# Optimization experiments

Hardware: AMD Instinct MI355X
Metric: run time of the kernel (lower is better)

Reference implementation:

```python
import jax, jax.numpy as jnp
import numpy as np

K = 3          # kernel size
STRIDE = 1
PAD = 1
GROUPS = 32    # GroupNorm groups
EPS = 1e-5


def setup_inputs() -> dict:
    key = jax.random.key(0)
    ks = jax.random.split(key, 6)
    B, Cin, H, W, Cout = 4, 256, 64, 64, 256
    K2 = K * K
    x = jax.random.normal(ks[0], (B, Cin, H, W), jnp.float32)
    offset = jax.random.normal(ks[1], (B, 2 * K2, H, W), jnp.float32)
    mask = jax.random.uniform(ks[2], (B, K2, H, W), jnp.float32)
    weight = jax.random.normal(ks[3], (Cout, Cin, K, K), jnp.float32) * (1.0 / np.sqrt(Cin * K2))
    bias = jnp.zeros((Cout,), jnp.float32)
    gamma = jnp.ones((Cout,), jnp.float32)   # constant_init(norm, 1)
    beta = jnp.zeros((Cout,), jnp.float32)   # bias=0
    return {"x": x, "offset": offset, "mask": mask, "weight": weight,
            "bias": bias, "gamma": gamma, "beta": beta}


def _modulated_deform_conv(x, offset, mask, weight, bias):
    """DCNv2: bilinear-sample x at learned offsets, modulate by mask, conv-accumulate."""
    B, Cin, H, W = x.shape
    Cout = weight.shape[0]
    K2 = K * K
    Ho = (H + 2 * PAD - K) // STRIDE + 1
    Wo = (W + 2 * PAD - K) // STRIDE + 1

    # base sampling grid per kernel point: [K2, Ho, Wo]
    ky, kx = jnp.meshgrid(jnp.arange(K), jnp.arange(K), indexing='ij')
    ky = ky.reshape(K2).astype(jnp.float32)
    kx = kx.reshape(K2).astype(jnp.float32)
    hs = (jnp.arange(Ho) * STRIDE - PAD).astype(jnp.float32)
    ws = (jnp.arange(Wo) * STRIDE - PAD).astype(jnp.float32)

    off = offset.reshape(B, K2, 2, Ho, Wo)  # interleaved (dy, dx) per kernel point
    y = ky[None, :, None, None] + hs[None, None, :, None] + off[:, :, 0]   # [B,K2,Ho,Wo]
    xc = kx[None, :, None, None] + ws[None, None, None, :] + off[:, :, 1]  # [B,K2,Ho,Wo]

    y0 = jnp.floor(y)
    x0 = jnp.floor(xc)
    dy = y - y0
    dx = xc - x0
    y0i = y0.astype(jnp.int32)
    x0i = x0.astype(jnp.int32)

    x_flat = x.reshape(B, Cin, H * W)

    def corner(yi, xi, w):
        # corner-wise zero padding outside the image (matches mmcv bilinear)
        valid = (yi >= 0) & (yi <= H - 1) & (xi >= 0) & (xi <= W - 1)
        idx = jnp.clip(yi, 0, H - 1) * W + jnp.clip(xi, 0, W - 1)  # [B,K2,Ho,Wo]
        idx_f = idx.reshape(B, -1)
        v = jax.vmap(lambda xf, i: xf[:, i])(x_flat, idx_f)  # [B, Cin, K2*Ho*Wo]
        wv = (w * valid.astype(w.dtype)).reshape(B, 1, -1)
        return v * wv

    val = (corner(y0i,     x0i,     (1 - dy) * (1 - dx))
         + corner(y0i,     x0i + 1, (1 - dy) * dx)
         + corner(y0i + 1, x0i,     dy * (1 - dx))
         + corner(y0i + 1, x0i + 1, dy * dx))
    val = val.reshape(B, Cin, K2, Ho, Wo) * mask[:, None]  # modulate

    w_r = weight.reshape(Cout, Cin, K2)
    out = jnp.einsum('bckhw,ock->bohw', val, w_r) + bias[None, :, None, None]
    return out


def _group_norm(x, gamma, beta):
    B, C, H, W = x.shape
    g = x.reshape(B, GROUPS, C // GROUPS, H, W)
    mu = g.mean(axis=(2, 3, 4), keepdims=True)
    var = ((g - mu) ** 2).mean(axis=(2, 3, 4), keepdims=True)
    g = (g - mu) * jax.lax.rsqrt(var + EPS)
    return g.reshape(B, C, H, W) * gamma[None, :, None, None] + beta[None, :, None, None]


def reference(x, offset, mask, weight, bias, gamma, beta):
    out = _modulated_deform_conv(x, offset, mask, weight, bias)
    out = _group_norm(out, gamma, beta)
    return jax.nn.relu(out)
```

## Files before the change

kernel.cpp:

```cpp
#include <hip/hip_runtime.h>
#include <math.h>

#define BB    4
#define CIN   256
#define HH    64
#define WWID  64
#define COUT  256
#define KKS   3
#define K2    9
#define PADV  1
#define HWSZ  4096
#define GROUPS 32
#define CPG   8
#define EPSV  1e-5f
#define KTOT  2304
#define ROWB  4608
#define NTOT  16384
#define NCHUNK 18

typedef __attribute__((ext_vector_type(8))) short bf16x8;
typedef __attribute__((ext_vector_type(4))) float f32x4;

#define GLOAD_LDS16(g, l) \
    __builtin_amdgcn_global_load_lds((const __attribute__((address_space(1))) unsigned int*)(g), \
                                     (__attribute__((address_space(3))) unsigned int*)(l), 16, 0, 0)

__device__ __forceinline__ unsigned short f2bf(float f) {
    unsigned u = __float_as_uint(f);
    u = (u + 0x7fffu + ((u >> 16) & 1u)) >> 16;
    return (unsigned short)u;
}
__device__ __forceinline__ float bflo(unsigned q) { return __uint_as_float(q << 16); }
__device__ __forceinline__ float bfhi(unsigned q) { return __uint_as_float(q & 0xffff0000u); }

__global__ __launch_bounds__(256)
void k_pre(const float* __restrict__ x, unsigned short* __restrict__ xh,
           const float* __restrict__ w, unsigned short* __restrict__ wtb,
           float* __restrict__ gstat) {
    int t = threadIdx.x;
    if (blockIdx.x < 128) {
        __shared__ float tile[32][33];
        int hw0 = blockIdx.x * 32;
        int c0  = blockIdx.y * 32;
        int b   = blockIdx.z;
        int tx = t & 31, ty = t >> 5;
        const float* xp = x + (size_t)b * CIN * HWSZ;
        #pragma unroll
        for (int i = 0; i < 4; i++)
            tile[ty + i * 8][tx] = xp[(c0 + ty + i * 8) * HWSZ + hw0 + tx];
        __syncthreads();
        int j = t >> 3, cq = t & 7;
        union { unsigned short s[4]; uint2 d; } pk;
        #pragma unroll
        for (int k = 0; k < 4; k++) pk.s[k] = f2bf(tile[cq * 4 + k][j]);
        *(uint2*)((char*)xh + ((size_t)b * HWSZ * CIN + (size_t)(hw0 + j) * CIN + c0 + cq * 4) * 2) = pk.d;
    } else {
        if (blockIdx.y == 0 && blockIdx.z == 0 && t < BB * GROUPS * 2) gstat[t] = 0.f;
        int idx = (blockIdx.y * 4 + blockIdx.z) * 256 + t;
        int co = idx >> 5, c8 = idx & 31;
        int cin0 = c8 * 8;
        for (int k2 = 0; k2 < K2; k2++) {
            union { unsigned short s[8]; uint4 q; } pk;
            #pragma unroll
            for (int j = 0; j < 8; j++)
                pk.s[j] = f2bf(w[(co * CIN + cin0 + j) * K2 + k2]);
            int phys = co * ROWB + k2 * 512 + (c8 >> 3) * 128 + ((c8 & 7) ^ (co & 7)) * 16;
            *(uint4*)((char*)wtb + phys) = pk.q;
        }
    }
}

__global__ __launch_bounds__(256)
void k_sample(const unsigned short* __restrict__ xh,
              const float* __restrict__ offset, const float* __restrict__ mask,
              unsigned short* __restrict__ val) {
    __shared__ int   cidx[16 * K2 * 4];
    __shared__ float cwgt[16 * K2 * 4];
    int n0 = blockIdx.x * 16;
    int b  = n0 >> 12;
    int t  = threadIdx.x;

    if (t < 16 * K2) {
        int p  = t / K2, k2 = t - p * K2;
        int hw = (n0 & 4095) + p;
        int ho = hw >> 6, wo = hw & 63;
        int ky = k2 / KKS, kx = k2 - ky * KKS;
        float dy = offset[((b * (2 * K2) + k2 * 2 + 0) * HWSZ) + hw];
        float dx = offset[((b * (2 * K2) + k2 * 2 + 1) * HWSZ) + hw];
        float m  = mask[(b * K2 + k2) * HWSZ + hw];
        float y  = (float)(ky + ho - PADV) + dy;
        float xc = (float)(kx + wo - PADV) + dx;
        float y0f = floorf(y), x0f = floorf(xc);
        float fy = y - y0f, fx = xc - x0f;
        int y0 = (int)y0f, x0 = (int)x0f;
        int   yy[2] = { y0, y0 + 1 };
        int   xx[2] = { x0, x0 + 1 };
        float wy[2] = { 1.f - fy, fy };
        float wx[2] = { 1.f - fx, fx };
        int base = t * 4;
        #pragma unroll
        for (int i = 0; i < 2; i++)
            #pragma unroll
            for (int j = 0; j < 2; j++) {
                int yi = yy[i], xi = xx[j];
                bool valid = (yi >= 0) && (yi < HH) && (xi >= 0) && (xi < WWID);
                int yc  = min(max(yi, 0), HH - 1);
                int xcc = min(max(xi, 0), WWID - 1);
                cidx[base + i * 2 + j] = yc * WWID + xcc;
                cwgt[base + i * 2 + j] = valid ? (wy[i] * wx[j] * m) : 0.f;
            }
    }
    __syncthreads();

    int c8 = t & 31, ps = t >> 5;
    const char* xb = (const char*)xh + (size_t)b * HWSZ * CIN * 2;
    #pragma unroll
    for (int i = 0; i < 2; i++) {
        int p = ps + 8 * i;
        int n = n0 + p;
        int skey = n & 7;
        for (int k2 = 0; k2 < K2; k2++) {
            int cb = (p * K2 + k2) * 4;
            float a0=0,a1=0,a2=0,a3=0,a4=0,a5=0,a6=0,a7=0;
            #pragma unroll
            for (int cor = 0; cor < 4; cor++) {
                float wv = cwgt[cb + cor];
                uint4 q = *(const uint4*)(xb + (size_t)cidx[cb + cor] * 512 + c8 * 16);
                a0 += wv * bflo(q.x); a1 += wv * bfhi(q.x);
                a2 += wv * bflo(q.y); a3 += wv * bfhi(q.y);
                a4 += wv * bflo(q.z); a5 += wv * bfhi(q.z);
                a6 += wv * bflo(q.w); a7 += wv * bfhi(q.w);
            }
            union { unsigned short s[8]; uint4 q; } pk;
            pk.s[0]=f2bf(a0); pk.s[1]=f2bf(a1); pk.s[2]=f2bf(a2); pk.s[3]=f2bf(a3);
            pk.s[4]=f2bf(a4); pk.s[5]=f2bf(a5); pk.s[6]=f2bf(a6); pk.s[7]=f2bf(a7);
            int phys = k2 * 512 + (c8 >> 3) * 128 + ((c8 & 7) ^ skey) * 16;
            *(uint4*)((char*)val + (size_t)n * ROWB + phys) = pk.q;
        }
    }
}

__global__ __launch_bounds__(256)
void k_gemm(const unsigned short* __restrict__ wtb, const unsigned short* __restrict__ val,
            const float* __restrict__ bias, float* __restrict__ out,
            float* __restrict__ gstat) {
    __shared__ unsigned short As[128 * 128];
    __shared__ unsigned short Bs[64 * 128];
    __shared__ float gs[16], gss[16];

    int m0 = blockIdx.x * 128, n0 = blockIdx.y * 64;
    int t = threadIdx.x, w = t >> 6, l = t & 63;
    int r16 = l & 15, half = l >> 4;
    int wm = w & 1, wn = w >> 1;
    int skey = r16 & 7;

    if (t < 16) { gs[t] = 0.f; gss[t] = 0.f; }

    const char* ag[8]; unsigned short* lA[8];
    const char* bg[4]; unsigned short* lB[4];
    #pragma unroll
    for (int i = 0; i < 8; i++) {
        int o = (w * 8 + i) * 64 + l;
        ag[i] = (const char*)wtb + (size_t)(m0 + (o >> 4)) * ROWB + (o & 15) * 16;
        lA[i] = (unsigned short*)As + (w * 8 + i) * 512;
    }
    #pragma unroll
    for (int i = 0; i < 4; i++) {
        int o = (w * 4 + i) * 64 + l;
        bg[i] = (const char*)val + (size_t)(n0 + (o >> 4)) * ROWB + (o & 15) * 16;
        lB[i] = (unsigned short*)Bs + (w * 4 + i) * 512;
    }

    f32x4 acc[4][2];
    #pragma unroll
    for (int mi = 0; mi < 4; mi++)
        #pragma unroll
        for (int ni = 0; ni < 2; ni++) acc[mi][ni] = (f32x4)0.f;

    for (int kc = 0; kc < NCHUNK; kc++) {
        #pragma unroll
        for (int i = 0; i < 8; i++) { GLOAD_LDS16(ag[i], lA[i]); ag[i] += 256; }
        #pragma unroll
        for (int i = 0; i < 4; i++) { GLOAD_LDS16(bg[i], lB[i]); bg[i] += 256; }
        __syncthreads();
        #pragma unroll
        for (int ks = 0; ks < 4; ks++) {
            int ks4 = ks * 4 + half;
            int up  = ((ks4 & 8) | ((ks4 & 7) ^ skey)) * 8;
            bf16x8 af[4], bfv[2];
            #pragma unroll
            for (int mi = 0; mi < 4; mi++)
                af[mi] = *(const bf16x8*)&As[(wm * 64 + mi * 16 + r16) * 128 + up];
            #pragma unroll
            for (int ni = 0; ni < 2; ni++)
                bfv[ni] = *(const bf16x8*)&Bs[(wn * 32 + ni * 16 + r16) * 128 + up];
            #pragma unroll
            for (int mi = 0; mi < 4; mi++)
                #pragma unroll
                for (int ni = 0; ni < 2; ni++)
                    acc[mi][ni] = __builtin_amdgcn_mfma_f32_16x16x32_bf16(
                        af[mi], bfv[ni], acc[mi][ni], 0, 0, 0);
        }
        __syncthreads();
    }

    int b = n0 >> 12;
    float s4[4] = {0,0,0,0}, ss4[4] = {0,0,0,0};
    #pragma unroll
    for (int mi = 0; mi < 4; mi++) {
        #pragma unroll
        for (int r = 0; r < 4; r++) {
            int co = m0 + wm * 64 + mi * 16 + half * 4 + r;
            float bs = bias[co];
            float* orow = out + ((size_t)(b * COUT + co)) * HWSZ;
            #pragma unroll
            for (int ni = 0; ni < 2; ni++) {
                int n = (n0 + wn * 32 + ni * 16 + r16) & 4095;
                float v = acc[mi][ni][r] + bs;
                orow[n] = v;
                s4[mi] += v; ss4[mi] += v * v;
            }
        }
    }
    int gb = half >> 1;
    #pragma unroll
    for (int mi = 0; mi < 4; mi++) {
        atomicAdd(&gs [wm * 8 + mi * 2 + gb], s4[mi]);
        atomicAdd(&gss[wm * 8 + mi * 2 + gb], ss4[mi]);
    }
    __syncthreads();
    if (t < 16) {
        int g = blockIdx.x * 16 + t;
        atomicAdd(&gstat[((b * GROUPS) + g) * 2 + 0], gs[t]);
        atomicAdd(&gstat[((b * GROUPS) + g) * 2 + 1], gss[t]);
    }
}

__global__ __launch_bounds__(256)
void k_gnfinal(float* __restrict__ out, const float* __restrict__ gstat,
               const float* __restrict__ gamma, const float* __restrict__ beta) {
    int i4 = blockIdx.x * 256 + threadIdx.x;
    int e  = i4 * 4;
    int c  = (e >> 12) & 255;
    int b  = e >> 20;
    int g  = c >> 3;
    float s  = gstat[((b * GROUPS) + g) * 2 + 0];
    float ss = gstat[((b * GROUPS) + g) * 2 + 1];
    const float inv = 1.f / (float)(CPG * HWSZ);
    float mu  = s * inv;
    float var = ss * inv - mu * mu;
    float rstd = rsqrtf(var + EPSV);
    float ga = gamma[c] * rstd;
    float be = beta[c] - mu * ga;
    float4 v = ((float4*)out)[i4];
    v.x = fmaxf(v.x * ga + be, 0.f);
    v.y = fmaxf(v.y * ga + be, 0.f);
    v.z = fmaxf(v.z * ga + be, 0.f);
    v.w = fmaxf(v.w * ga + be, 0.f);
    ((float4*)out)[i4] = v;
}

extern "C" void kernel_launch(void* const* d_in, const int* in_sizes, int n_in,
                              void* d_out, int out_size, void* d_ws, size_t ws_size,
                              hipStream_t stream) {
    const float* x      = (const float*)d_in[0];
    const float* offset = (const float*)d_in[1];
    const float* mask   = (const float*)d_in[2];
    const float* weight = (const float*)d_in[3];
    const float* bias   = (const float*)d_in[4];
    const float* gamma  = (const float*)d_in[5];
    const float* beta   = (const float*)d_in[6];
    float* out = (float*)d_out;

    unsigned short* xh    = (unsigned short*)d_ws;
    unsigned short* wtb   = xh + (size_t)4194304;
    unsigned short* val   = wtb + (size_t)589824;
    float*          gstat = (float*)(val + (size_t)37748736);

    k_pre<<<dim3(129, 8, 4), 256, 0, stream>>>(x, xh, weight, wtb, gstat);
    k_sample<<<NTOT / 16, 256, 0, stream>>>(xh, offset, mask, val);
    k_gemm<<<dim3(2, 256), 256, 0, stream>>>(wtb, val, bias, out, gstat);
    k_gnfinal<<<(size_t)BB * COUT * HWSZ / 1024, 256, 0, stream>>>(out, gstat, gamma, beta);
}
```

Before: 151.4 us.

## Fuse GEMM and GroupNorm finalize via cooperative grid sync, rework swizzle

Merges the GEMM and the GroupNorm/ReLU pass into one cooperative kernel. Accumulators stay in registers across a grid-wide sync, then each block reads the finished group statistics and writes normalized output once. This removes one full write and read of the output tensor and one kernel launch. It also changes the LDS swizzle to XOR the 16-chunk index with the row parity, and batches the sampling kernel's gathers across two pixels for more memory-level parallelism. The grid sync needs all 512 blocks resident at once (two per CU by launch bounds) and costs a global barrier.

```diff
diff --git a/kernel.cpp b/kernel.cpp
--- a/kernel.cpp
+++ b/kernel.cpp
@@ -1,5 +1,8 @@
 #include <hip/hip_runtime.h>
+#include <hip/hip_cooperative_groups.h>
 #include <math.h>
+
+namespace cg = cooperative_groups;
 
 #define BB    4
 #define CIN   256
@@ -32,6 +35,13 @@
 }
 __device__ __forceinline__ float bflo(unsigned q) { return __uint_as_float(q << 16); }
 __device__ __forceinline__ float bfhi(unsigned q) { return __uint_as_float(q & 0xffff0000u); }
+__device__ __forceinline__ float aload(const float* p) {
+    return __hip_atomic_load(p, __ATOMIC_RELAXED, __HIP_MEMORY_SCOPE_AGENT);
+}
+
+__device__ __forceinline__ int physchunk(int c, int row) {
+    return ((c & 7) ^ (row & 7)) | ((c & 8) ^ ((row & 1) << 3));
+}
 
 __global__ __launch_bounds__(256)
 void k_pre(const float* __restrict__ x, unsigned short* __restrict__ xh,
@@ -59,12 +69,14 @@
         int idx = (blockIdx.y * 4 + blockIdx.z) * 256 + t;
         int co = idx >> 5, c8 = idx & 31;
         int cin0 = c8 * 8;
+        int w2 = c8 >> 4, c = c8 & 15;
+        int pc = physchunk(c, co);
         for (int k2 = 0; k2 < K2; k2++) {
             union { unsigned short s[8]; uint4 q; } pk;
             #pragma unroll
             for (int j = 0; j < 8; j++)
                 pk.s[j] = f2bf(w[(co * CIN + cin0 + j) * K2 + k2]);
-            int phys = co * ROWB + k2 * 512 + (c8 >> 3) * 128 + ((c8 & 7) ^ (co & 7)) * 16;
+            int phys = co * ROWB + k2 * 512 + w2 * 256 + pc * 16;
             *(uint4*)((char*)wtb + phys) = pk.q;
         }
     }
@@ -114,36 +126,51 @@
 
     int c8 = t & 31, ps = t >> 5;
     const char* xb = (const char*)xh + (size_t)b * HWSZ * CIN * 2;
-    #pragma unroll
-    for (int i = 0; i < 2; i++) {
-        int p = ps + 8 * i;
-        int n = n0 + p;
-        int skey = n & 7;
-        for (int k2 = 0; k2 < K2; k2++) {
-            int cb = (p * K2 + k2) * 4;
+    int w2 = c8 >> 4, cc = c8 & 15;
+    int nA = n0 + ps, nB = n0 + ps + 8;
+    int pcA = physchunk(cc, nA), pcB = physchunk(cc, nB);
+
+    #pragma unroll 2
+    for (int k2 = 0; k2 < K2; k2++) {
+        int cb0 = (ps * K2 + k2) * 4;
+        int cb1 = ((ps + 8) * K2 + k2) * 4;
+        uint4 q[2][4]; float wv[2][4];
+        #pragma unroll
+        for (int cor = 0; cor < 4; cor++) {
+            wv[0][cor] = cwgt[cb0 + cor];
+            q[0][cor]  = *(const uint4*)(xb + (size_t)cidx[cb0 + cor] * 512 + c8 * 16);
+        }
+        #pragma unroll
+        for (int cor = 0; cor < 4; cor++) {
+            wv[1][cor] = cwgt[cb1 + cor];
+            q[1][cor]  = *(const uint4*)(xb + (size_t)cidx[cb1 + cor] * 512 + c8 * 16);
+        }
+        #pragma unroll
+        for (int i = 0; i < 2; i++) {
             float a0=0,a1=0,a2=0,a3=0,a4=0,a5=0,a6=0,a7=0;
             #pragma unroll
             for (int cor = 0; cor < 4; cor++) {
-                float wv = cwgt[cb + cor];
-                uint4 q = *(const uint4*)(xb + (size_t)cidx[cb + cor] * 512 + c8 * 16);
-                a0 += wv * bflo(q.x); a1 += wv * bfhi(q.x);
-                a2 += wv * bflo(q.y); a3 += wv * bfhi(q.y);
-                a4 += wv * bflo(q.z); a5 += wv * bfhi(q.z);
-                a6 += wv * bflo(q.w); a7 += wv * bfhi(q.w);
+                float wvv = wv[i][cor]; uint4 qq = q[i][cor];
+                a0 += wvv * bflo(qq.x); a1 += wvv * bfhi(qq.x);
+                a2 += wvv * bflo(qq.y); a3 += wvv * bfhi(qq.y);
+                a4 += wvv * bflo(qq.z); a5 += wvv * bfhi(qq.z);
+                a6 += wvv * bflo(qq.w); a7 += wvv * bfhi(qq.w);
             }
             union { unsigned short s[8]; uint4 q; } pk;
             pk.s[0]=f2bf(a0); pk.s[1]=f2bf(a1); pk.s[2]=f2bf(a2); pk.s[3]=f2bf(a3);
             pk.s[4]=f2bf(a4); pk.s[5]=f2bf(a5); pk.s[6]=f2bf(a6); pk.s[7]=f2bf(a7);
-            int phys = k2 * 512 + (c8 >> 3) * 128 + ((c8 & 7) ^ skey) * 16;
-            *(uint4*)((char*)val + (size_t)n * ROWB + phys) = pk.q;
-        }
-    }
-}
-
-__global__ __launch_bounds__(256)
-void k_gemm(const unsigned short* __restrict__ wtb, const unsigned short* __restrict__ val,
-            const float* __restrict__ bias, float* __restrict__ out,
-            float* __restrict__ gstat) {
+            int n  = i ? nB : nA;
+            int pc = i ? pcB : pcA;
+            *(uint4*)((char*)val + (size_t)n * ROWB + k2 * 512 + w2 * 256 + pc * 16) = pk.q;
+        }
+    }
+}
+
+__global__ __launch_bounds__(256, 2)
+void k_gemmfin(const unsigned short* __restrict__ wtb, const unsigned short* __restrict__ val,
+               const float* __restrict__ bias, const float* __restrict__ gamma,
+               const float* __restrict__ beta, float* __restrict__ out,
+               float* __restrict__ gstat) {
     __shared__ unsigned short As[128 * 128];
     __shared__ unsigned short Bs[64 * 128];
     __shared__ float gs[16], gss[16];
@@ -152,7 +179,6 @@
     int t = threadIdx.x, w = t >> 6, l = t & 63;
     int r16 = l & 15, half = l >> 4;
     int wm = w & 1, wn = w >> 1;
-    int skey = r16 & 7;
 
     if (t < 16) { gs[t] = 0.f; gss[t] = 0.f; }
 
@@ -186,7 +212,7 @@
         #pragma unroll
         for (int ks = 0; ks < 4; ks++) {
             int ks4 = ks * 4 + half;
-            int up  = ((ks4 & 8) | ((ks4 & 7) ^ skey)) * 8;
+            int up  = physchunk(ks4, r16) * 8;
             bf16x8 af[4], bfv[2];
             #pragma unroll
             for (int mi = 0; mi < 4; mi++)
@@ -210,14 +236,11 @@
     for (int mi = 0; mi < 4; mi++) {
         #pragma unroll
         for (int r = 0; r < 4; r++) {
-            int co = m0 + wm * 64 + mi * 16 + half * 4 + r;
-            float bs = bias[co];
-            float* orow = out + ((size_t)(b * COUT + co)) * HWSZ;
+            float bs = bias[m0 + wm * 64 + mi * 16 + half * 4 + r];
             #pragma unroll
             for (int ni = 0; ni < 2; ni++) {
-                int n = (n0 + wn * 32 + ni * 16 + r16) & 4095;
                 float v = acc[mi][ni][r] + bs;
-                orow[n] = v;
+                acc[mi][ni][r] = v;
                 s4[mi] += v; ss4[mi] += v * v;
             }
         }
@@ -234,30 +257,31 @@
         atomicAdd(&gstat[((b * GROUPS) + g) * 2 + 0], gs[t]);
         atomicAdd(&gstat[((b * GROUPS) + g) * 2 + 1], gss[t]);
     }
-}
-
-__global__ __launch_bounds__(256)
-void k_gnfinal(float* __restrict__ out, const float* __restrict__ gstat,
-               const float* __restrict__ gamma, const float* __restrict__ beta) {
-    int i4 = blockIdx.x * 256 + threadIdx.x;
-    int e  = i4 * 4;
-    int c  = (e >> 12) & 255;
-    int b  = e >> 20;
-    int g  = c >> 3;
-    float s  = gstat[((b * GROUPS) + g) * 2 + 0];
-    float ss = gstat[((b * GROUPS) + g) * 2 + 1];
+
+    cg::this_grid().sync();
+
     const float inv = 1.f / (float)(CPG * HWSZ);
-    float mu  = s * inv;
-    float var = ss * inv - mu * mu;
-    float rstd = rsqrtf(var + EPSV);
-    float ga = gamma[c] * rstd;
-    float be = beta[c] - mu * ga;
-    float4 v = ((float4*)out)[i4];
-    v.x = fmaxf(v.x * ga + be, 0.f);
-    v.y = fmaxf(v.y * ga + be, 0.f);
-    v.z = fmaxf(v.z * ga + be, 0.f);
-    v.w = fmaxf(v.w * ga + be, 0.f);
-    ((float4*)out)[i4] = v;
+    #pragma unroll
+    for (int mi = 0; mi < 4; mi++) {
+        int g = ((m0 + wm * 64 + mi * 16) >> 3) + gb;
+        float s  = aload(&gstat[((b * GROUPS) + g) * 2 + 0]);
+        float ss = aload(&gstat[((b * GROUPS) + g) * 2 + 1]);
+        float mu  = s * inv;
+        float var = ss * inv - mu * mu;
+        float rstd = rsqrtf(var + EPSV);
+        #pragma unroll
+        for (int r = 0; r < 4; r++) {
+            int co = m0 + wm * 64 + mi * 16 + half * 4 + r;
+            float ga = gamma[co] * rstd;
+            float be = beta[co] - mu * ga;
+            float* orow = out + ((size_t)(b * COUT + co)) * HWSZ;
+            #pragma unroll
+            for (int ni = 0; ni < 2; ni++) {
+                int n = (n0 + wn * 32 + ni * 16 + r16) & 4095;
+                orow[n] = fmaxf(acc[mi][ni][r] * ga + be, 0.f);
+            }
+        }
+    }
 }
 
 extern "C" void kernel_launch(void* const* d_in, const int* in_sizes, int n_in,
@@ -279,6 +303,10 @@
 
     k_pre<<<dim3(129, 8, 4), 256, 0, stream>>>(x, xh, weight, wtb, gstat);
     k_sample<<<NTOT / 16, 256, 0, stream>>>(xh, offset, mask, val);
-    k_gemm<<<dim3(2, 256), 256, 0, stream>>>(wtb, val, bias, out, gstat);
-    k_gnfinal<<<(size_t)BB * COUT * HWSZ / 1024, 256, 0, stream>>>(out, gstat, gamma, beta);
-}
+
+    const unsigned short* wtb_c = wtb; const unsigned short* val_c = val;
+    void* args[] = { (void*)&wtb_c, (void*)&val_c, (void*)&bias, (void*)&gamma,
+                     (void*)&beta, (void*)&out, (void*)&gstat };
+    hipLaunchCooperativeKernel((void*)k_gemmfin, dim3(2, 256), dim3(256),
+                               args, 0, stream);
+}
```

After: 207.6 us. 37.1% more time.

## Fuse deformable bilinear sampling into GEMM B-tile production, drop val buffer

Applied to the files above, without the earlier changes.

Removes the separate sampling kernel that wrote a large bf16 im2col-style val matrix to global memory. The GEMM now computes corner indices and weights for its 64 pixels into shared memory, then builds each K-chunk of the B tile in LDS from gathered xh rows. The swizzle is changed to a new physchunk pattern that covers all 16 chunks. This saves a large global write and read plus a kernel launch. In exchange, the sampling gathers are repeated by both M-blocks (gridDim.x=2), and the synchronous gathers sit in the GEMM inner loop, which may expose latency.

```diff
diff --git a/kernel.cpp b/kernel.cpp
--- a/kernel.cpp
+++ b/kernel.cpp
@@ -33,6 +33,17 @@
 __device__ __forceinline__ float bflo(unsigned q) { return __uint_as_float(q << 16); }
 __device__ __forceinline__ float bfhi(unsigned q) { return __uint_as_float(q & 0xffff0000u); }
 
+__device__ __forceinline__ int physchunk(int c, int row) {
+    return ((c & 7) ^ (row & 7)) | ((c & 8) ^ ((row & 1) << 3));
+}
+
+__device__ __forceinline__ void fma8(float* f, float w, uint4 q) {
+    f[0] += w * bflo(q.x); f[1] += w * bfhi(q.x);
+    f[2] += w * bflo(q.y); f[3] += w * bfhi(q.y);
+    f[4] += w * bflo(q.z); f[5] += w * bfhi(q.z);
+    f[6] += w * bflo(q.w); f[7] += w * bfhi(q.w);
+}
+
 __global__ __launch_bounds__(256)
 void k_pre(const float* __restrict__ x, unsigned short* __restrict__ xh,
            const float* __restrict__ w, unsigned short* __restrict__ wtb,
@@ -59,30 +70,41 @@
         int idx = (blockIdx.y * 4 + blockIdx.z) * 256 + t;
         int co = idx >> 5, c8 = idx & 31;
         int cin0 = c8 * 8;
+        int w2 = c8 >> 4, c = c8 & 15;
+        int pc = physchunk(c, co);
         for (int k2 = 0; k2 < K2; k2++) {
             union { unsigned short s[8]; uint4 q; } pk;
             #pragma unroll
             for (int j = 0; j < 8; j++)
                 pk.s[j] = f2bf(w[(co * CIN + cin0 + j) * K2 + k2]);
-            int phys = co * ROWB + k2 * 512 + (c8 >> 3) * 128 + ((c8 & 7) ^ (co & 7)) * 16;
+            int phys = co * ROWB + k2 * 512 + w2 * 256 + pc * 16;
             *(uint4*)((char*)wtb + phys) = pk.q;
         }
     }
 }
 
 __global__ __launch_bounds__(256)
-void k_sample(const unsigned short* __restrict__ xh,
-              const float* __restrict__ offset, const float* __restrict__ mask,
-              unsigned short* __restrict__ val) {
-    __shared__ int   cidx[16 * K2 * 4];
-    __shared__ float cwgt[16 * K2 * 4];
-    int n0 = blockIdx.x * 16;
-    int b  = n0 >> 12;
-    int t  = threadIdx.x;
-
-    if (t < 16 * K2) {
-        int p  = t / K2, k2 = t - p * K2;
-        int hw = (n0 & 4095) + p;
+void k_gemm(const unsigned short* __restrict__ wtb, const unsigned short* __restrict__ xh,
+            const float* __restrict__ offset, const float* __restrict__ mask,
+            const float* __restrict__ bias, float* __restrict__ out,
+            float* __restrict__ gstat) {
+    __shared__ unsigned short As[128 * 128];
+    __shared__ unsigned short Bs[64 * 128];
+    __shared__ int   cidx[64 * K2 * 4];
+    __shared__ float cwgt[64 * K2 * 4];
+    __shared__ float gs[16], gss[16];
+
+    int m0 = blockIdx.x * 128, n0 = blockIdx.y * 64;
+    int b = n0 >> 12;
+    int t = threadIdx.x, w = t >> 6, l = t & 63;
+    int r16 = l & 15, half = l >> 4;
+    int wm = w & 1, wn = w >> 1;
+
+    if (t < 16) { gs[t] = 0.f; gss[t] = 0.f; }
+
+    for (int i = t; i < 64 * K2; i += 256) {
+        int px = i / K2, k2 = i - px * K2;
+        int hw = (n0 & 4095) + px;
         int ho = hw >> 6, wo = hw & 63;
         int ky = k2 / KKS, kx = k2 - ky * KKS;
         float dy = offset[((b * (2 * K2) + k2 * 2 + 0) * HWSZ) + hw];
@@ -97,79 +119,30 @@
         int   xx[2] = { x0, x0 + 1 };
         float wy[2] = { 1.f - fy, fy };
         float wx[2] = { 1.f - fx, fx };
-        int base = t * 4;
-        #pragma unroll
-        for (int i = 0; i < 2; i++)
-            #pragma unroll
-            for (int j = 0; j < 2; j++) {
-                int yi = yy[i], xi = xx[j];
+        #pragma unroll
+        for (int ii = 0; ii < 2; ii++)
+            #pragma unroll
+            for (int jj = 0; jj < 2; jj++) {
+                int yi = yy[ii], xi = xx[jj];
                 bool valid = (yi >= 0) && (yi < HH) && (xi >= 0) && (xi < WWID);
                 int yc  = min(max(yi, 0), HH - 1);
                 int xcc = min(max(xi, 0), WWID - 1);
-                cidx[base + i * 2 + j] = yc * WWID + xcc;
-                cwgt[base + i * 2 + j] = valid ? (wy[i] * wx[j] * m) : 0.f;
+                cidx[i * 4 + ii * 2 + jj] = yc * WWID + xcc;
+                cwgt[i * 4 + ii * 2 + jj] = valid ? (wy[ii] * wx[jj] * m) : 0.f;
             }
     }
-    __syncthreads();
-
-    int c8 = t & 31, ps = t >> 5;
-    const char* xb = (const char*)xh + (size_t)b * HWSZ * CIN * 2;
-    #pragma unroll
-    for (int i = 0; i < 2; i++) {
-        int p = ps + 8 * i;
-        int n = n0 + p;
-        int skey = n & 7;
-        for (int k2 = 0; k2 < K2; k2++) {
-            int cb = (p * K2 + k2) * 4;
-            float a0=0,a1=0,a2=0,a3=0,a4=0,a5=0,a6=0,a7=0;
-            #pragma unroll
-            for (int cor = 0; cor < 4; cor++) {
-                float wv = cwgt[cb + cor];
-                uint4 q = *(const uint4*)(xb + (size_t)cidx[cb + cor] * 512 + c8 * 16);
-                a0 += wv * bflo(q.x); a1 += wv * bfhi(q.x);
-                a2 += wv * bflo(q.y); a3 += wv * bfhi(q.y);
-                a4 += wv * bflo(q.z); a5 += wv * bfhi(q.z);
-                a6 += wv * bflo(q.w); a7 += wv * bfhi(q.w);
-            }
-            union { unsigned short s[8]; uint4 q; } pk;
-            pk.s[0]=f2bf(a0); pk.s[1]=f2bf(a1); pk.s[2]=f2bf(a2); pk.s[3]=f2bf(a3);
-            pk.s[4]=f2bf(a4); pk.s[5]=f2bf(a5); pk.s[6]=f2bf(a6); pk.s[7]=f2bf(a7);
-            int phys = k2 * 512 + (c8 >> 3) * 128 + ((c8 & 7) ^ skey) * 16;
-            *(uint4*)((char*)val + (size_t)n * ROWB + phys) = pk.q;
-        }
-    }
-}
-
-__global__ __launch_bounds__(256)
-void k_gemm(const unsigned short* __restrict__ wtb, const unsigned short* __restrict__ val,
-            const float* __restrict__ bias, float* __restrict__ out,
-            float* __restrict__ gstat) {
-    __shared__ unsigned short As[128 * 128];
-    __shared__ unsigned short Bs[64 * 128];
-    __shared__ float gs[16], gss[16];
-
-    int m0 = blockIdx.x * 128, n0 = blockIdx.y * 64;
-    int t = threadIdx.x, w = t >> 6, l = t & 63;
-    int r16 = l & 15, half = l >> 4;
-    int wm = w & 1, wn = w >> 1;
-    int skey = r16 & 7;
-
-    if (t < 16) { gs[t] = 0.f; gss[t] = 0.f; }
 
     const char* ag[8]; unsigned short* lA[8];
-    const char* bg[4]; unsigned short* lB[4];
     #pragma unroll
     for (int i = 0; i < 8; i++) {
         int o = (w * 8 + i) * 64 + l;
         ag[i] = (const char*)wtb + (size_t)(m0 + (o >> 4)) * ROWB + (o & 15) * 16;
         lA[i] = (unsigned short*)As + (w * 8 + i) * 512;
     }
-    #pragma unroll
-    for (int i = 0; i < 4; i++) {
-        int o = (w * 4 + i) * 64 + l;
-        bg[i] = (const char*)val + (size_t)(n0 + (o >> 4)) * ROWB + (o & 15) * 16;
-        lB[i] = (unsigned short*)Bs + (w * 4 + i) * 512;
-    }
+
+    int sc  = t & 15;
+    int tpx = t >> 4;
+    const char* xb = (const char*)xh + (size_t)b * HWSZ * CIN * 2;
 
     f32x4 acc[4][2];
     #pragma unroll
@@ -177,16 +150,42 @@
         #pragma unroll
         for (int ni = 0; ni < 2; ni++) acc[mi][ni] = (f32x4)0.f;
 
+    __syncthreads();
+
     for (int kc = 0; kc < NCHUNK; kc++) {
         #pragma unroll
         for (int i = 0; i < 8; i++) { GLOAD_LDS16(ag[i], lA[i]); ag[i] += 256; }
-        #pragma unroll
-        for (int i = 0; i < 4; i++) { GLOAD_LDS16(bg[i], lB[i]); bg[i] += 256; }
+
+        int k2 = kc >> 1, h = kc & 1;
+        const char* xbs = xb + h * 256 + sc * 16;
+        uint4 g[4][4];
+        #pragma unroll
+        for (int ps = 0; ps < 4; ps++) {
+            int cb = ((ps * 16 + tpx) * K2 + k2) * 4;
+            #pragma unroll
+            for (int c = 0; c < 4; c++)
+                g[ps][c] = *(const uint4*)(xbs + (size_t)cidx[cb + c] * 512);
+        }
+        #pragma unroll
+        for (int ps = 0; ps < 4; ps++) {
+            int px = ps * 16 + tpx;
+            int cb = (px * K2 + k2) * 4;
+            float f[8] = {0,0,0,0,0,0,0,0};
+            fma8(f, cwgt[cb + 0], g[ps][0]);
+            fma8(f, cwgt[cb + 1], g[ps][1]);
+            fma8(f, cwgt[cb + 2], g[ps][2]);
+            fma8(f, cwgt[cb + 3], g[ps][3]);
+            union { unsigned short s[8]; uint4 q; } pk;
+            #pragma unroll
+            for (int e = 0; e < 8; e++) pk.s[e] = f2bf(f[e]);
+            *(uint4*)&Bs[px * 128 + physchunk(sc, px) * 8] = pk.q;
+        }
         __syncthreads();
+
         #pragma unroll
         for (int ks = 0; ks < 4; ks++) {
             int ks4 = ks * 4 + half;
-            int up  = ((ks4 & 8) | ((ks4 & 7) ^ skey)) * 8;
+            int up  = physchunk(ks4, r16) * 8;
             bf16x8 af[4], bfv[2];
             #pragma unroll
             for (int mi = 0; mi < 4; mi++)
@@ -204,7 +203,6 @@
         __syncthreads();
     }
 
-    int b = n0 >> 12;
     float s4[4] = {0,0,0,0}, ss4[4] = {0,0,0,0};
     #pragma unroll
     for (int mi = 0; mi < 4; mi++) {
@@ -274,11 +272,9 @@
 
     unsigned short* xh    = (unsigned short*)d_ws;
     unsigned short* wtb   = xh + (size_t)4194304;
-    unsigned short* val   = wtb + (size_t)589824;
-    float*          gstat = (float*)(val + (size_t)37748736);
+    float*          gstat = (float*)(wtb + (size_t)589824);
 
     k_pre<<<dim3(129, 8, 4), 256, 0, stream>>>(x, xh, weight, wtb, gstat);
-    k_sample<<<NTOT / 16, 256, 0, stream>>>(xh, offset, mask, val);
-    k_gemm<<<dim3(2, 256), 256, 0, stream>>>(wtb, val, bias, out, gstat);
+    k_gemm<<<dim3(2, 256), 256, 0, stream>>>(wtb, xh, offset, mask, bias, out, gstat);
     k_gnfinal<<<(size_t)BB * COUT * HWSZ / 1024, 256, 0, stream>>>(out, gstat, gamma, beta);
 }
```

Measured after the change: 162.2 us. 1.07x slower.
